# Kernel tuning notes

Measured on AMD Instinct MI355X. Metric: run time of the kernel, lower is better.

The kernel has to match this reference:

```python
import jax, jax.numpy as jnp
import numpy as np

H = 512  # hidden size per direction


def _sru_layer(x, W, wc, b):
    # x: (L, B, n_in). Bidirectional SRU layer, identity activation (sru pkg default).
    L, B, n_in = x.shape
    k = W.shape[1] // (2 * H)  # 4 if n_in != 2H (projected highway) else 3
    U = (x @ W).reshape(L, B, 2, k, H)  # (L,B,dir,k,H)
    vf, vr = wc.reshape(2, 2, H)        # peephole vectors, (dir,H) each
    bf, br = b.reshape(2, 2, H)
    # put dir axis at 1 and reverse time for the backward direction
    Ud = jnp.stack([U[:, :, 0], jnp.flip(U[:, :, 1], axis=0)], axis=1)  # (L,2,B,k,H)

    def step(c, u):  # c: (2,B,H), u: (2,B,k,H)
        f = jax.nn.sigmoid(u[:, :, 1] + vf[:, None] * c + bf[:, None])
        c = f * c + (1.0 - f) * u[:, :, 0]
        return c, c

    c0 = jnp.zeros((2, B, H), x.dtype)
    _, c_seq = jax.lax.scan(step, c0, Ud)  # (L,2,B,H)
    r = jax.nn.sigmoid(Ud[:, :, :, 2] + vr[None, :, None] * c_seq + br[None, :, None])
    if k == 4:
        res = Ud[:, :, :, 3]
    else:
        xr = x.reshape(L, B, 2, H)
        res = jnp.stack([xr[:, :, 0], jnp.flip(xr[:, :, 1], axis=0)], axis=1)
    h = r * c_seq + (1.0 - r) * res  # (L,2,B,H)
    h_fwd = h[:, 0]
    h_bwd = jnp.flip(h[:, 1], axis=0)
    return jnp.concatenate([h_fwd, h_bwd], axis=-1)  # (L,B,2H)


def setup_inputs() -> dict:
    key = jax.random.key(0)
    ks = iter(jax.random.split(key, 20))
    B, L = 8, 2048
    inp = {"X": jax.random.normal(next(ks), (B, L, 1), jnp.float32)}
    n_in = 1
    for i in range(4):
        k = 4 if n_in != 2 * H else 3
        inp[f"W{i}"] = jax.random.normal(next(ks), (n_in, 2 * k * H), jnp.float32) / np.float32(np.sqrt(max(n_in, 1)))
        inp[f"wc{i}"] = jax.random.normal(next(ks), (4 * H,), jnp.float32) * 0.1
        inp[f"b{i}"] = jnp.zeros((4 * H,), jnp.float32)
        n_in = 2 * H
    inp["Wcls"] = jax.random.normal(next(ks), (2 * H, 3), jnp.float32) * 0.02
    inp["bcls"] = jnp.zeros((3,), jnp.float32)
    return inp


def reference(X, W0, wc0, b0, W1, wc1, b1, W2, wc2, b2, W3, wc3, b3, Wcls, bcls):
    # first-difference along time, zeroing t=0 (X -= X.roll(1,1); X[:,0] *= 0)
    dX = X - jnp.roll(X, 1, axis=1)
    dX = dX.at[:, 0].set(0.0)
    x = jnp.transpose(dX, (1, 0, 2))  # (L,B,1)
    for W, wc, b in ((W0, wc0, b0), (W1, wc1, b1), (W2, wc2, b2), (W3, wc3, b3)):
        x = _sru_layer(x, W, wc, b)
    y = jnp.transpose(x, (1, 0, 2))  # (B,L,2H)
    return y @ Wcls + bcls
```

## Files before the change

kernel.cpp:

```cpp
#include <hip/hip_runtime.h>
#include <hip/hip_bf16.h>

typedef __hip_bfloat16 bf16;
typedef unsigned short u16x8 __attribute__((ext_vector_type(8)));
using v8s = __attribute__((ext_vector_type(8))) short;
using v4f = __attribute__((ext_vector_type(4))) float;

#define L_SEQ 2048
#define BATCH 8
#define NIN   1024
#define WLD   3072
#define NHALF 1536
#define NROWS (L_SEQ*BATCH)
#define L2E   1.4426950408889634f

__device__ __forceinline__ float bits2f(unsigned short u){ return __uint_as_float(((unsigned)u)<<16); }
__device__ __forceinline__ float b2f(bf16 v){ return __bfloat162float(v); }
__device__ __forceinline__ bf16  f2b(float v){ return __float2bfloat16(v); }

__device__ __forceinline__ void gload16(const void* g, void* l){
    __builtin_amdgcn_global_load_lds((const __attribute__((address_space(1))) void*)g,
                                     (__attribute__((address_space(3))) void*)l, 16, 0, 0);
}

__global__ void k_code(float* __restrict__ out, float v){
    if (threadIdx.x == 0 && blockIdx.x == 0) out[0] = v;
}

__global__ __launch_bounds__(256) void k_diff(const float* __restrict__ X, float* __restrict__ dxT){
    int i = blockIdx.x*256 + threadIdx.x;
    if (i >= NROWS) return;
    int l = i & (L_SEQ-1);
    float v = 0.f;
    if (l > 0) v = X[i] - X[i-1];
    dxT[i] = v;
}

__global__ __launch_bounds__(256) void k_wt(const float* __restrict__ W, bf16* __restrict__ Wt){
    __shared__ float t[32][33];
    int k0 = blockIdx.x*32, n0 = blockIdx.y*32;
    int tx = threadIdx.x & 31, ty = threadIdx.x >> 5;
    #pragma unroll
    for (int j=0;j<4;j++)
        t[ty*4+j][tx] = W[(size_t)(k0+ty*4+j)*WLD + n0 + tx];
    __syncthreads();
    #pragma unroll
    for (int j=0;j<4;j++)
        Wt[(size_t)(n0+ty*4+j)*NIN + k0 + tx] = f2b(t[tx][ty*4+j]);
}

__global__ __launch_bounds__(256) void k_layer0(const float* __restrict__ dxT, const float* __restrict__ W0,
                                                const float* __restrict__ wc, const float* __restrict__ bb,
                                                bf16* __restrict__ xout){
    __shared__ float sdx[L_SEQ];
    int g = blockIdx.x*256 + threadIdx.x;
    int h = g & 511, b = (g>>9) & 7, d = g >> 12;
    const float* dxp = dxT + b*L_SEQ;
    for (int t = threadIdx.x; t < L_SEQ; t += 256) sdx[t] = dxp[t];
    __syncthreads();

    int dcol = d*512 + h;
    float w0  = W0[d*2048 + h];
    float w1L = W0[d*2048 + 512 + h]*L2E;
    float w2L = W0[d*2048 + 1024 + h]*L2E;
    float w3  = W0[d*2048 + 1536 + h];
    float vfL = wc[dcol]*L2E,  vrL = wc[1024 + dcol]*L2E;
    float bfvL = bb[dcol]*L2E, brvL = bb[1024 + dcol]*L2E;
    float c = 0.f;

    int t0 = d ? (L_SEQ-1) : 0;
    bf16* xq = xout + ((size_t)t0*BATCH + b)*NIN + dcol;
    ptrdiff_t xs = d ? -(ptrdiff_t)(BATCH*NIN) : (ptrdiff_t)(BATCH*NIN);

#define LD0(P0,P1,P2,P3, s0) do{                                     \
        _Pragma("unroll")                                            \
        for (int i_=0;i_<8;i_++){                                    \
            int ss_ = (s0)+i_;                                       \
            float xv_ = sdx[d ? (L_SEQ-1-ss_) : ss_];                \
            P0[i_] = xv_*w0;                                         \
            P1[i_] = fmaf(xv_, w1L, bfvL);                           \
            P2[i_] = fmaf(xv_, w2L, brvL);                           \
            P3[i_] = xv_*w3;                                         \
        }                                                            \
        __builtin_amdgcn_sched_barrier(0);                           \
    }while(0)

#define STEP8(P0,P1,P2,P3) do{                                       \
        float cs_[8];                                                \
        _Pragma("unroll")                                            \
        for (int i_=0;i_<8;i_++){                                    \
            float e_ = exp2f(fmaf(-vfL, c, -P1[i_]));                \
            float f_ = __builtin_amdgcn_rcpf(1.f + e_);              \
            c = fmaf(f_, c - P0[i_], P0[i_]);                        \
            cs_[i_] = c;                                             \
        }                                                            \
        __builtin_amdgcn_sched_barrier(0);                           \
        _Pragma("unroll")                                            \
        for (int i_=0;i_<8;i_++){                                    \
            float e2_ = exp2f(fmaf(-vrL, cs_[i_], -P2[i_]));         \
            float r_ = __builtin_amdgcn_rcpf(1.f + e2_);             \
            xq[(ptrdiff_t)i_*xs] = f2b(fmaf(r_, cs_[i_]-P3[i_], P3[i_])); \
        }                                                            \
        xq += 8*xs;                                                  \
        __builtin_amdgcn_sched_barrier(0);                           \
    }while(0)

    float A0[8],A1[8],A2[8],A3[8], B0[8],B1[8],B2[8],B3[8];
    LD0(A0,A1,A2,A3, 0);
    for (int s0 = 0; s0 + 32 <= L_SEQ; s0 += 16){
        LD0(B0,B1,B2,B3, s0+8);
        STEP8(A0,A1,A2,A3);
        LD0(A0,A1,A2,A3, s0+16);
        STEP8(B0,B1,B2,B3);
    }
    LD0(B0,B1,B2,B3, L_SEQ-8);
    STEP8(A0,A1,A2,A3);
    STEP8(B0,B1,B2,B3);
#undef LD0
#undef STEP8
}

__global__ __launch_bounds__(256) void k_gemm(const bf16* __restrict__ Xin, const bf16* __restrict__ Wt,
                                              bf16* __restrict__ Uc, int l0, int C){
    __shared__ bf16 As[3][4096];
    __shared__ bf16 Bs[3][4096];
    int tid = threadIdx.x;
    int lane = tid & 63;
    int s = blockIdx.z;
    int base = (s == 0) ? l0 : (L_SEQ - l0 - C);
    const bf16* A  = Xin + (size_t)base*BATCH*NIN;
    const bf16* Bm = Wt + (size_t)s*NHALF*NIN;
    bf16*       Cc = Uc + (size_t)s*(size_t)C*BATCH*NHALF;

    int m0 = blockIdx.x*128, n0 = blockIdx.y*128;
    int wv = tid >> 6;
    int wm = (wv >> 1)*64, wn = (wv & 1)*64;

    v4f acc[4][4];
    #pragma unroll
    for (int i=0;i<4;i++)
        #pragma unroll
        for (int j=0;j<4;j++)
            #pragma unroll
            for (int r=0;r<4;r++) acc[i][j][r] = 0.f;

    int row_a = tid >> 2;
    int kb = (((tid & 3) ^ ((tid >> 3) & 3)))*8;
    int wbase = (tid & 192)*16;
    int fro = (lane & 15)*64 + (((lane >> 4) ^ (((lane & 15) >> 1) & 3)))*16;

#define STAGE(q, k0) do{                                                        \
        char* la_ = (char*)As[0] + (q)*8192;                                    \
        char* lb_ = (char*)Bs[0] + (q)*8192;                                    \
        gload16(A  + (size_t)(m0 + row_a      )*NIN + (k0) + kb, la_ + wbase);  \
        gload16(A  + (size_t)(m0 + row_a + 64 )*NIN + (k0) + kb, la_ + 4096 + wbase); \
        gload16(Bm + (size_t)(n0 + row_a      )*NIN + (k0) + kb, lb_ + wbase);  \
        gload16(Bm + (size_t)(n0 + row_a + 64 )*NIN + (k0) + kb, lb_ + 4096 + wbase); \
    }while(0)

    STAGE(0, 0);
    STAGE(1, 32);
    int cur = 0;
    for (int it = 0; it < 32; ++it){
        if (it < 30){
            int nb = cur + 2; if (nb >= 3) nb -= 3;
            STAGE(nb, (it+2)*32);
            asm volatile("s_waitcnt vmcnt(8)" ::: "memory");
        } else if (it == 30){
            asm volatile("s_waitcnt vmcnt(4)" ::: "memory");
        } else {
            asm volatile("s_waitcnt vmcnt(0)" ::: "memory");
        }
        __builtin_amdgcn_sched_barrier(0);
        __builtin_amdgcn_s_barrier();
        const char* la = (const char*)As[0] + cur*8192;
        const char* lb = (const char*)Bs[0] + cur*8192;
        v8s av[4], bv[4];
        #pragma unroll
        for (int i=0;i<4;i++) av[i] = *(const v8s*)(la + (wm + i*16)*64 + fro);
        #pragma unroll
        for (int j=0;j<4;j++) bv[j] = *(const v8s*)(lb + (wn + j*16)*64 + fro);
        #pragma unroll
        for (int i=0;i<4;i++)
            #pragma unroll
            for (int j=0;j<4;j++)
                acc[i][j] = __builtin_amdgcn_mfma_f32_16x16x32_bf16(av[i], bv[j], acc[i][j], 0, 0, 0);
        __builtin_amdgcn_s_barrier();
        cur = cur + 1; if (cur == 3) cur = 0;
    }
#undef STAGE

    int cr = (lane >> 4)*4, ccol = lane & 15;
    #pragma unroll
    for (int i=0;i<4;i++){
        #pragma unroll
        for (int j=0;j<4;j++){
            size_t rb = (size_t)(m0 + wm + i*16 + cr)*NHALF + (n0 + wn + j*16 + ccol);
            #pragma unroll
            for (int r=0;r<4;r++) Cc[rb + (size_t)r*NHALF] = f2b(acc[i][j][r]);
        }
    }
}

__global__ __launch_bounds__(128) void k_rec(const bf16* __restrict__ Uc, const bf16* __restrict__ xin,
                                             bf16* __restrict__ xout, float* __restrict__ carry,
                                             const float* __restrict__ wc, const float* __restrict__ bb,
                                             int l0, int C){
    __shared__ bf16  Ub[3][3072];
    __shared__ bf16  Xb[3][1024];
    __shared__ float csb[2][1024];
    int tid = threadIdx.x;
    int wv = tid >> 6, lane = tid & 63;
    int bid = blockIdx.x;
    int d = bid >> 6, b = (bid >> 3) & 7, hbase = (bid & 7)*64;
    int h = hbase + lane;
    int dcol = d*512 + h;
    int ch = d*4096 + b*512 + h;
    float vfL = wc[d*512 + h]*L2E, vrL = wc[1024 + d*512 + h]*L2E;
    float bfvL = bb[d*512 + h]*L2E, brvL = bb[1024 + d*512 + h]*L2E;
    float c = (l0 == 0) ? 0.f : carry[ch];

    const bf16* Ubase = Uc + (size_t)d*(size_t)C*12288 + b*1536 + hbase;
    int lo3 = lane >> 3, ci8 = (lane & 7)*8;
    int ngrp = C >> 4;

#define RST_W0(base_, q_) do{                                                   \
        char* ub_ = (char*)Ub[q_];                                              \
        _Pragma("unroll")                                                       \
        for (int qq=0; qq<3; ++qq){                                             \
            int seg = qq*8 + lo3;                                               \
            int st_ = seg/3, gate_ = seg - st_*3;                               \
            int ss_ = (base_) + st_;                                            \
            int row_ = d ? (C-1-ss_) : ss_;                                     \
            gload16(Ubase + (size_t)row_*12288 + gate_*512 + ci8,               \
                    ub_ + qq*1024);                                             \
        }                                                                       \
    }while(0)

#define RST_W1(base_, q_) do{                                                   \
        char* ub_ = (char*)Ub[q_]; char* xb_ = (char*)Xb[q_];                   \
        _Pragma("unroll")                                                       \
        for (int qq=3; qq<6; ++qq){                                             \
            int seg = qq*8 + lo3;                                               \
            int st_ = seg/3, gate_ = seg - st_*3;                               \
            int ss_ = (base_) + st_;                                            \
            int row_ = d ? (C-1-ss_) : ss_;                                     \
            gload16(Ubase + (size_t)row_*12288 + gate_*512 + ci8,               \
                    ub_ + qq*1024);                                             \
        }                                                                       \
        _Pragma("unroll")                                                       \
        for (int j=0;j<2;++j){                                                  \
            int st_ = (base_) + j*8 + lo3;                                      \
            int t_  = d ? (L_SEQ-1 - l0 - st_) : (l0 + st_);                    \
            gload16(xin + ((size_t)t_*BATCH + b)*NIN + d*512 + hbase + ci8,     \
                    xb_ + j*1024);                                              \
        }                                                                       \
    }while(0)

#define DSR(dst, o) asm volatile("ds_read_u16 %0, %1 offset:" #o : "=v"(dst) : "v"(ab))

#define CHAIN(q_, qc_) do{                                                      \
        unsigned ab = (unsigned)(size_t)&Ub[q_][lane];                          \
        unsigned t0_[16], t1_[16];                                              \
        DSR(t0_[0] ,0);    DSR(t1_[0] ,128);                                    \
        DSR(t0_[1] ,384);  DSR(t1_[1] ,512);                                    \
        DSR(t0_[2] ,768);  DSR(t1_[2] ,896);                                    \
        DSR(t0_[3] ,1152); DSR(t1_[3] ,1280);                                   \
        DSR(t0_[4] ,1536); DSR(t1_[4] ,1664);                                   \
        DSR(t0_[5] ,1920); DSR(t1_[5] ,2048);                                   \
        DSR(t0_[6] ,2304); DSR(t1_[6] ,2432);                                   \
        DSR(t0_[7] ,2688); DSR(t1_[7] ,2816);                                   \
        DSR(t0_[8] ,3072); DSR(t1_[8] ,3200);                                   \
        DSR(t0_[9] ,3456); DSR(t1_[9] ,3584);                                   \
        DSR(t0_[10],3840); DSR(t1_[10],3968);                                   \
        DSR(t0_[11],4224); DSR(t1_[11],4352);                                   \
        DSR(t0_[12],4608); DSR(t1_[12],4736);                                   \
        DSR(t0_[13],4992); DSR(t1_[13],5120);                                   \
        DSR(t0_[14],5376); DSR(t1_[14],5504);                                   \
        DSR(t0_[15],5760); DSR(t1_[15],5888);                                   \
        asm volatile("s_waitcnt lgkmcnt(0)" ::: "memory");                      \
        __builtin_amdgcn_sched_barrier(0);                                      \
        _Pragma("unroll")                                                       \
        for (int i_=0;i_<16;i_++){                                              \
            float u0_ = __uint_as_float(t0_[i_]<<16);                           \
            float u1L_= fmaf(__uint_as_float(t1_[i_]<<16), L2E, bfvL);          \
            float e_ = exp2f(fmaf(-vfL, c, -u1L_));                             \
            float f_ = __builtin_amdgcn_rcpf(1.f + e_);                         \
            c = fmaf(f_, c - u0_, u0_);                                         \
            csb[qc_][i_*64 + lane] = c;                                         \
        }                                                                       \
    }while(0)

#define POST(gp_, qp_, qcp_) do{                                                \
        bf16* xq_ = xout + ((size_t)(d ? (L_SEQ-1 - l0 - (gp_)*16) : (l0 + (gp_)*16))*BATCH + b)*NIN + dcol; \
        ptrdiff_t xs_ = d ? -(ptrdiff_t)(BATCH*NIN) : (ptrdiff_t)(BATCH*NIN);   \
        _Pragma("unroll")                                                       \
        for (int i_=0;i_<16;i_++){                                              \
            float cs_ = csb[qcp_][i_*64 + lane];                                \
            float u2L_ = fmaf(b2f(Ub[qp_][(i_*3+2)*64 + lane]), L2E, brvL);     \
            float xr_  = b2f(Xb[qp_][i_*64 + lane]);                            \
            float e2_ = exp2f(fmaf(-vrL, cs_, -u2L_));                          \
            float r_ = __builtin_amdgcn_rcpf(1.f + e2_);                        \
            xq_[(ptrdiff_t)i_*xs_] = f2b(fmaf(r_, cs_-xr_, xr_));               \
        }                                                                       \
    }while(0)

    if (wv == 0) RST_W0(0, 0); else RST_W1(0, 0);
    asm volatile("s_waitcnt vmcnt(0)" ::: "memory");
    __builtin_amdgcn_sched_barrier(0);
    __builtin_amdgcn_s_barrier();

    int q0 = 0;
    for (int g = 0; g < ngrp; ++g){
        int qn = q0 + 1; if (qn == 3) qn = 0;
        if (g + 1 < ngrp){
            if (wv == 0){
                RST_W0((g+1)*16, qn);
                asm volatile("s_waitcnt vmcnt(3)" ::: "memory");
            } else {
                RST_W1((g+1)*16, qn);
                if (g < 2) asm volatile("s_waitcnt vmcnt(5)" ::: "memory");
                else       asm volatile("s_waitcnt vmcnt(21)" ::: "memory");
            }
        } else {
            if (wv == 0) asm volatile("s_waitcnt vmcnt(0)" ::: "memory");
            else         asm volatile("s_waitcnt vmcnt(16)" ::: "memory");
        }
        __builtin_amdgcn_sched_barrier(0);
        __builtin_amdgcn_s_barrier();

        if (wv == 0){
            CHAIN(q0, g & 1);
        } else if (g > 0){
            int qp = q0 + 2; if (qp >= 3) qp -= 3;
            POST(g-1, qp, (g-1) & 1);
        }
        __builtin_amdgcn_sched_barrier(0);
        asm volatile("s_waitcnt lgkmcnt(0)" ::: "memory");
        __builtin_amdgcn_sched_barrier(0);
        __builtin_amdgcn_s_barrier();
        q0 = qn;
    }
    if (wv == 1){
        int qp = q0 + 2; if (qp >= 3) qp -= 3;
        POST(ngrp-1, qp, (ngrp-1) & 1);
    } else {
        carry[ch] = c;
    }
#undef RST_W0
#undef RST_W1
#undef CHAIN
#undef POST
#undef DSR
}

__global__ __launch_bounds__(256) void k_cls(const bf16* __restrict__ Xf, const float* __restrict__ Wc,
                                             const float* __restrict__ bc, float* __restrict__ out){
    int wave = threadIdx.x >> 6, lane = threadIdx.x & 63;
    int row = blockIdx.x*4 + wave;
    const bf16* xp = Xf + (size_t)row*NIN + lane*16;
    u16x8 v0 = *(const u16x8*)(xp);
    u16x8 v1 = *(const u16x8*)(xp + 8);
    float a0=0.f, a1=0.f, a2=0.f;
    #pragma unroll
    for (int i=0;i<16;i++){
        float xv = bits2f(i<8 ? v0[i&7] : v1[i&7]);
        int k = lane*16 + i;
        a0 += xv*Wc[k*3+0];
        a1 += xv*Wc[k*3+1];
        a2 += xv*Wc[k*3+2];
    }
    #pragma unroll
    for (int off=32; off; off>>=1){
        a0 += __shfl_down(a0, off);
        a1 += __shfl_down(a1, off);
        a2 += __shfl_down(a2, off);
    }
    if (lane == 0){
        int l = row >> 3, b = row & 7;
        float* op = out + ((size_t)b*L_SEQ + l)*3;
        op[0] = a0 + bc[0];
        op[1] = a1 + bc[1];
        op[2] = a2 + bc[2];
    }
}

extern "C" void kernel_launch(void* const* d_in, const int* in_sizes, int n_in,
                              void* d_out, int out_size, void* d_ws, size_t ws_size,
                              hipStream_t stream){
    (void)in_sizes; (void)n_in; (void)out_size;
    const float* X    = (const float*)d_in[0];
    const float* W[4]  = {(const float*)d_in[1],(const float*)d_in[4],(const float*)d_in[7],(const float*)d_in[10]};
    const float* wc[4] = {(const float*)d_in[2],(const float*)d_in[5],(const float*)d_in[8],(const float*)d_in[11]};
    const float* bb[4] = {(const float*)d_in[3],(const float*)d_in[6],(const float*)d_in[9],(const float*)d_in[12]};
    const float* Wcls = (const float*)d_in[13];
    const float* bcls = (const float*)d_in[14];
    float* out = (float*)d_out;

    char*  ws    = (char*)d_ws;
    bf16*  xA    = (bf16*)ws;
    bf16*  xB    = (bf16*)(ws + 33554432);
    float* dxT   = (float*)(ws + 67108864);
    float* carry = (float*)(ws + 67174400);
    bf16*  Wt[3] = {(bf16*)(ws + 67207168), (bf16*)(ws + 73498624), (bf16*)(ws + 79790080)};
    bf16*  Ucb   = (bf16*)(ws + 86081536);
    const size_t NEEDED = 86081536ull + 64ull*49152ull;

    if (ws_size < NEEDED){
        float code = 1.0e6f + (float)((ws_size >> 20) > 9999 ? 9999 : (ws_size >> 20)) * 100.0f;
        k_code<<<1, 64, 0, stream>>>(out, code);
        return;
    }

    int C = 2048;
    while (C > 64 && 86081536ull + (size_t)C*49152ull > ws_size) C >>= 1;

    k_diff  <<<(NROWS+255)/256, 256, 0, stream>>>(X, dxT);
    for (int i = 0; i < 3; ++i)
        k_wt<<<dim3(32,96), 256, 0, stream>>>(W[i+1], Wt[i]);
    k_layer0<<<32, 256, 0, stream>>>(dxT, W[0], wc[0], bb[0], xA);

    bf16* xin = xA; bf16* xo = xB;
    for (int layer = 1; layer < 4; ++layer){
        for (int l0 = 0; l0 < L_SEQ; l0 += C){
            dim3 g(C*8/128, NHALF/128, 2);
            k_gemm<<<g, 256, 0, stream>>>(xin, Wt[layer-1], Ucb, l0, C);
            k_rec <<<128, 128, 0, stream>>>(Ucb, xin, xo, carry, wc[layer], bb[layer], l0, C);
        }
        bf16* t = xin; xin = xo; xo = t;
    }
    k_cls<<<NROWS/4, 256, 0, stream>>>(xin, Wcls, bcls, out);
}
```

Baseline: 1.016 ms.

## Split layer0 recurrence and output gating across producer/consumer wavefronts

Layer 0's kernel now runs 128 blocks of two wavefronts instead of 32 blocks of four. In each block, wavefront 0 runs only the serial forget-gate recurrence for 16 steps at a time and writes the c values to a double-buffered LDS array. Wavefront 1 computes the reset gate and highway output for the previous group, synchronised by a block barrier each group. This takes the reset-gate math and global stores off the serial critical path and spreads the work over more CUs, at the cost of 128 barriers and LDS traffic.

```diff
diff --git a/kernel.cpp b/kernel.cpp
--- a/kernel.cpp
+++ b/kernel.cpp
@@ -49,17 +49,21 @@
         Wt[(size_t)(n0+ty*4+j)*NIN + k0 + tx] = f2b(t[tx][ty*4+j]);
 }
 
-__global__ __launch_bounds__(256) void k_layer0(const float* __restrict__ dxT, const float* __restrict__ W0,
+__global__ __launch_bounds__(128) void k_layer0(const float* __restrict__ dxT, const float* __restrict__ W0,
                                                 const float* __restrict__ wc, const float* __restrict__ bb,
                                                 bf16* __restrict__ xout){
     __shared__ float sdx[L_SEQ];
-    int g = blockIdx.x*256 + threadIdx.x;
-    int h = g & 511, b = (g>>9) & 7, d = g >> 12;
+    __shared__ float csb[2][1024];
+    int tid = threadIdx.x;
+    int wv = tid >> 6, lane = tid & 63;
+    int bid = blockIdx.x;
+    int d = bid >> 6, b = (bid >> 3) & 7, hbase = (bid & 7)*64;
+    int h = hbase + lane;
+    int dcol = d*512 + h;
     const float* dxp = dxT + b*L_SEQ;
-    for (int t = threadIdx.x; t < L_SEQ; t += 256) sdx[t] = dxp[t];
+    for (int t = tid; t < L_SEQ; t += 128) sdx[t] = dxp[t];
     __syncthreads();
 
-    int dcol = d*512 + h;
     float w0  = W0[d*2048 + h];
     float w1L = W0[d*2048 + 512 + h]*L2E;
     float w2L = W0[d*2048 + 1024 + h]*L2E;
@@ -67,57 +71,47 @@
     float vfL = wc[dcol]*L2E,  vrL = wc[1024 + dcol]*L2E;
     float bfvL = bb[dcol]*L2E, brvL = bb[1024 + dcol]*L2E;
     float c = 0.f;
-
-    int t0 = d ? (L_SEQ-1) : 0;
-    bf16* xq = xout + ((size_t)t0*BATCH + b)*NIN + dcol;
     ptrdiff_t xs = d ? -(ptrdiff_t)(BATCH*NIN) : (ptrdiff_t)(BATCH*NIN);
 
-#define LD0(P0,P1,P2,P3, s0) do{                                     \
-        _Pragma("unroll")                                            \
-        for (int i_=0;i_<8;i_++){                                    \
-            int ss_ = (s0)+i_;                                       \
-            float xv_ = sdx[d ? (L_SEQ-1-ss_) : ss_];                \
-            P0[i_] = xv_*w0;                                         \
-            P1[i_] = fmaf(xv_, w1L, bfvL);                           \
-            P2[i_] = fmaf(xv_, w2L, brvL);                           \
-            P3[i_] = xv_*w3;                                         \
-        }                                                            \
-        __builtin_amdgcn_sched_barrier(0);                           \
-    }while(0)
-
-#define STEP8(P0,P1,P2,P3) do{                                       \
-        float cs_[8];                                                \
-        _Pragma("unroll")                                            \
-        for (int i_=0;i_<8;i_++){                                    \
-            float e_ = exp2f(fmaf(-vfL, c, -P1[i_]));                \
-            float f_ = __builtin_amdgcn_rcpf(1.f + e_);              \
-            c = fmaf(f_, c - P0[i_], P0[i_]);                        \
-            cs_[i_] = c;                                             \
-        }                                                            \
-        __builtin_amdgcn_sched_barrier(0);                           \
-        _Pragma("unroll")                                            \
-        for (int i_=0;i_<8;i_++){                                    \
-            float e2_ = exp2f(fmaf(-vrL, cs_[i_], -P2[i_]));         \
-            float r_ = __builtin_amdgcn_rcpf(1.f + e2_);             \
-            xq[(ptrdiff_t)i_*xs] = f2b(fmaf(r_, cs_[i_]-P3[i_], P3[i_])); \
-        }                                                            \
-        xq += 8*xs;                                                  \
-        __builtin_amdgcn_sched_barrier(0);                           \
-    }while(0)
-
-    float A0[8],A1[8],A2[8],A3[8], B0[8],B1[8],B2[8],B3[8];
-    LD0(A0,A1,A2,A3, 0);
-    for (int s0 = 0; s0 + 32 <= L_SEQ; s0 += 16){
-        LD0(B0,B1,B2,B3, s0+8);
-        STEP8(A0,A1,A2,A3);
-        LD0(A0,A1,A2,A3, s0+16);
-        STEP8(B0,B1,B2,B3);
-    }
-    LD0(B0,B1,B2,B3, L_SEQ-8);
-    STEP8(A0,A1,A2,A3);
-    STEP8(B0,B1,B2,B3);
-#undef LD0
-#undef STEP8
+#define L0POST(gp_) do{                                                         \
+        int s0_ = (gp_)*16;                                                     \
+        bf16* xq_ = xout + ((size_t)(d ? (L_SEQ-1-s0_) : s0_)*BATCH + b)*NIN + dcol; \
+        _Pragma("unroll")                                                       \
+        for (int i_=0;i_<16;i_++){                                              \
+            int s_ = s0_ + i_;                                                  \
+            float xv_ = sdx[d ? (L_SEQ-1-s_) : s_];                             \
+            float cs_ = csb[(gp_) & 1][i_*64 + lane];                           \
+            float P2_ = fmaf(xv_, w2L, brvL);                                   \
+            float P3_ = xv_*w3;                                                 \
+            float e2_ = exp2f(fmaf(-vrL, cs_, -P2_));                           \
+            float r_ = __builtin_amdgcn_rcpf(1.f + e2_);                        \
+            xq_[(ptrdiff_t)i_*xs] = f2b(fmaf(r_, cs_ - P3_, P3_));              \
+        }                                                                       \
+    }while(0)
+
+    for (int g = 0; g < 128; ++g){
+        if (wv == 0){
+            #pragma unroll
+            for (int i = 0; i < 16; ++i){
+                int s = g*16 + i;
+                float xv = sdx[d ? (L_SEQ-1-s) : s];
+                float P0 = xv*w0;
+                float P1 = fmaf(xv, w1L, bfvL);
+                float e = exp2f(fmaf(-vfL, c, -P1));
+                float f = __builtin_amdgcn_rcpf(1.f + e);
+                c = fmaf(f, c - P0, P0);
+                csb[g & 1][i*64 + lane] = c;
+            }
+        } else if (g > 0){
+            L0POST(g-1);
+        }
+        __builtin_amdgcn_sched_barrier(0);
+        asm volatile("s_waitcnt lgkmcnt(0)" ::: "memory");
+        __builtin_amdgcn_sched_barrier(0);
+        __builtin_amdgcn_s_barrier();
+    }
+    if (wv == 1) L0POST(127);
+#undef L0POST
 }
 
 __global__ __launch_bounds__(256) void k_gemm(const bf16* __restrict__ Xin, const bf16* __restrict__ Wt,
@@ -418,7 +412,7 @@
     k_diff  <<<(NROWS+255)/256, 256, 0, stream>>>(X, dxT);
     for (int i = 0; i < 3; ++i)
         k_wt<<<dim3(32,96), 256, 0, stream>>>(W[i+1], Wt[i]);
-    k_layer0<<<32, 256, 0, stream>>>(dxT, W[0], wc[0], bb[0], xA);
+    k_layer0<<<128, 128, 0, stream>>>(dxT, W[0], wc[0], bb[0], xA);
 
     bf16* xin = xA; bf16* xo = xB;
     for (int layer = 1; layer < 4; ++layer){
```

Result: faster. 960.1 us (-5.5%).
